# Kernel optimization log

Hardware: AMD Instinct MI355X
Metric: run time of the kernel (lower is better)

## Reference

```python
import jax, jax.numpy as jnp
import numpy as np
from math import sqrt

B, L, H, DK = 4, 2048, 16, 64


def setup_inputs() -> dict:
    key = jax.random.key(0)
    kq, kk, kv = jax.random.split(key, 3)
    queries = jax.random.normal(kq, (B, L, H, DK), dtype=jnp.float32)
    keys = jax.random.normal(kk, (B, L, H, DK), dtype=jnp.float32)
    values = jax.random.normal(kv, (B, L, H, DK), dtype=jnp.float32)
    return {"queries": queries, "keys": keys, "values": values}


def reference(queries, keys, values):
    # FullAttention forward: mask_flag=True, scale=None -> 1/sqrt(dk),
    # attention_dropout=0.0 (identity), output_attention=False.
    b, l, h, dk = queries.shape
    s = values.shape[1]
    scale = 1.0 / sqrt(dk)
    # scores: [B, H, L, S]
    scores = jnp.einsum('blhd,bshd->bhls', queries, keys)
    # causal mask: upper triangle (strictly above diagonal) -> -inf
    causal = jnp.triu(jnp.ones((l, s), dtype=bool), k=1)  # [L, S]
    scores = jnp.where(causal[None, None, :, :], -jnp.inf, scores)
    attn = jax.nn.softmax(scores * scale, axis=-1)
    out = jnp.einsum('bhls,bshd->blhd', attn, values)
    return out
```

## Files before the change

kernel.cpp:

```cpp
#include <hip/hip_runtime.h>
#include <hip/hip_bf16.h>
#include <cstdint>
#include <cstddef>

#define B_ 4
#define L_ 2048
#define H_ 16
#define D_ 64
#define BH_ (B_*H_)

typedef __attribute__((ext_vector_type(8))) short short8;
typedef __attribute__((ext_vector_type(4))) short short4_t;
typedef __attribute__((ext_vector_type(4))) float f32x4;

__device__ __forceinline__ short f2bf(float x) {
    union { float f; unsigned u; } v; v.f = x;
    unsigned r = v.u + 0x7fffu + ((v.u >> 16) & 1u);
    return (short)(r >> 16);
}

__device__ __forceinline__ short8 pack8(float4 a, float4 b, float sc) {
    short8 t;
    t[0] = f2bf(a.x * sc); t[1] = f2bf(a.y * sc);
    t[2] = f2bf(a.z * sc); t[3] = f2bf(a.w * sc);
    t[4] = f2bf(b.x * sc); t[5] = f2bf(b.y * sc);
    t[6] = f2bf(b.z * sc); t[7] = f2bf(b.w * sc);
    return t;
}

__device__ __forceinline__ float fast_exp2(float x) {
#if __has_builtin(__builtin_amdgcn_exp2f)
    return __builtin_amdgcn_exp2f(x);
#else
    return exp2f(x);
#endif
}

__device__ __forceinline__ void gld16(const void* g, void* l) {
    __builtin_amdgcn_global_load_lds(
        (const __attribute__((address_space(1))) void*)g,
        (__attribute__((address_space(3))) void*)l, 16, 0, 0);
}

__global__ __launch_bounds__(256) void prepack(
    const float* __restrict__ K, const float* __restrict__ V,
    short* __restrict__ Kb, short* __restrict__ Vt)
{
    const int blk = blockIdx.x;
    const int bh  = blk >> 5;
    const int s0  = (blk & 31) * 64;
    const int b   = bh >> 4, h = bh & 15;
    const int t   = threadIdx.x;
    __shared__ short Ls[64 * 72];

#pragma unroll
    for (int half = 0; half < 2; ++half) {
        const int sl = (t >> 3) + half * 32;
        const int dc = (t & 7) * 8;
        const size_t src_off = ((size_t)((b * L_ + s0 + sl) * H_ + h)) * D_ + dc;
        float4 f0 = *(const float4*)(K + src_off);
        float4 f1 = *(const float4*)(K + src_off + 4);
        *(short8*)&Kb[((size_t)bh * L_ + s0 + sl) * D_ + dc] = pack8(f0, f1, 1.0f);
        float4 g0 = *(const float4*)(V + src_off);
        float4 g1 = *(const float4*)(V + src_off + 4);
        *(short8*)&Ls[sl * 72 + dc] = pack8(g0, g1, 1.0f);
    }
    __syncthreads();
    const int d  = t >> 2;
    const int sc = (t & 3) * 16;
    short8 o0, o1;
#pragma unroll
    for (int j = 0; j < 8; ++j) o0[j] = Ls[(sc + j) * 72 + d];
#pragma unroll
    for (int j = 0; j < 8; ++j) o1[j] = Ls[(sc + 8 + j) * 72 + d];
    short* dst = Vt + ((size_t)bh * D_ + d) * L_ + s0 + sc;
    *(short8*)dst = o0;
    *(short8*)(dst + 8) = o1;
}

__global__ __launch_bounds__(256, 4) void fa_fwd2(
    const float* __restrict__ Q, const short* __restrict__ Kb,
    const short* __restrict__ Vt, float* __restrict__ O)
{
    const int tid  = threadIdx.x;
    const int wave = tid >> 6;
    const int lane = tid & 63;
    const int quad = lane >> 4;
    const int l16  = lane & 15;

    const int blk  = blockIdx.x;
    const int xcd  = blk & 7;
    const int slot = blk >> 3;
    const int bh   = xcd * 8 + (slot & 7);
    const int ip   = slot >> 3;
    const int b    = bh >> 4;
    const int h    = bh & 15;
    const int qtA  = ip;
    const int qtB  = 31 - ip;
    const int qbA  = qtA * 64;
    const int qbB  = qtB * 64;
    const int nkt  = qtB + 1;

    __shared__ short Ks[2][64 * 64];
    __shared__ short Vs[2][64 * 64];
    __shared__ short Ps[4][16 * 64];
    short* Pl = Ps[wave];

    const float scq = 0.125f * 1.44269504f;
    short8 qfA[2], qfB[2];
    {
        const float* qa = Q + ((size_t)((b * L_ + qbA + wave * 16 + l16) * H_ + h)) * D_;
        const float* qb = Q + ((size_t)((b * L_ + qbB + wave * 16 + l16) * H_ + h)) * D_;
#pragma unroll
        for (int kk = 0; kk < 2; ++kk) {
            const int d0 = kk * 32 + quad * 8;
            qfA[kk] = pack8(*(const float4*)(qa + d0), *(const float4*)(qa + d0 + 4), scq);
            qfB[kk] = pack8(*(const float4*)(qb + d0), *(const float4*)(qb + d0 + 4), scq);
        }
    }

    const short* Kg = Kb + (size_t)bh * L_ * D_;
    const short* Vg = Vt + (size_t)bh * D_ * L_;
    const int r8 = lane >> 3;
    const int g8 = ((lane & 7) ^ r8) * 8;

    f32x4 accA[4], accB[4];
#pragma unroll
    for (int c = 0; c < 4; ++c) {
        accA[c] = (f32x4){0.f, 0.f, 0.f, 0.f};
        accB[c] = (f32x4){0.f, 0.f, 0.f, 0.f};
    }
    float lsA[4] = {0.f, 0.f, 0.f, 0.f};
    float lsB[4] = {0.f, 0.f, 0.f, 0.f};

    auto stage = [&](int kt, int buf) {
#pragma unroll
        for (int half = 0; half < 2; ++half) {
            const int rbase = wave * 16 + half * 8;
            const int row   = rbase + r8;
            gld16(Kg + (size_t)(kt * 64 + row) * D_ + g8, &Ks[buf][rbase * 64]);
            gld16(Vg + (size_t)row * L_ + kt * 64 + g8, &Vs[buf][rbase * 64]);
        }
    };

    auto compute = [&](int kt, int buf, const short8* qf, int qt, f32x4* acc, float* ls) {
        f32x4 s[4];
#pragma unroll
        for (int ct = 0; ct < 4; ++ct) s[ct] = (f32x4){0.f, 0.f, 0.f, 0.f};
#pragma unroll
        for (int kk = 0; kk < 2; ++kk) {
            const int cs = ((kk * 4 + quad) ^ (l16 & 7)) * 8;
#pragma unroll
            for (int ct = 0; ct < 4; ++ct) {
                short8 kf = *(short8*)&Ks[buf][(ct * 16 + l16) * 64 + cs];
                s[ct] = __builtin_amdgcn_mfma_f32_16x16x32_bf16(qf[kk], kf, s[ct], 0, 0, 0);
            }
        }
        const bool diag = (kt == qt);
#pragma unroll
        for (int ct = 0; ct < 4; ++ct) {
#pragma unroll
            for (int r = 0; r < 4; ++r) {
                float sv = s[ct][r];
                if (diag && (ct * 16 + l16 > wave * 16 + quad * 4 + r)) sv = -1e30f;
                const float p = fast_exp2(sv);
                ls[r] += p;
                const int row = quad * 4 + r, col = ct * 16 + l16;
                Pl[row * 64 + ((col >> 3) ^ (row & 7)) * 8 + (col & 7)] = f2bf(p);
            }
        }
#pragma unroll
        for (int ks = 0; ks < 2; ++ks) {
            const int cs = ((ks * 4 + quad) ^ (l16 & 7)) * 8;
            short8 pa = *(short8*)&Pl[l16 * 64 + cs];
#pragma unroll
            for (int cd = 0; cd < 4; ++cd) {
                short8 vb = *(short8*)&Vs[buf][(cd * 16 + l16) * 64 + cs];
                acc[cd] = __builtin_amdgcn_mfma_f32_16x16x32_bf16(pa, vb, acc[cd], 0, 0, 0);
            }
        }
    };

    stage(0, 0);
    __syncthreads();
    for (int kt = 0; kt < nkt; ++kt) {
        const int buf = kt & 1;
        if (kt + 1 < nkt) stage(kt + 1, buf ^ 1);
        if (kt <= qtA) compute(kt, buf, qfA, qtA, accA, lsA);
        compute(kt, buf, qfB, qtB, accB, lsB);
        __syncthreads();
    }

    auto epi = [&](int qbX, f32x4* acc, float* ls) {
#pragma unroll
        for (int r = 0; r < 4; ++r) {
            float t = ls[r];
#pragma unroll
            for (int off = 1; off < 16; off <<= 1) t += __shfl_xor(t, off);
            const float inv = 1.0f / t;
            float* orow = O + ((size_t)((b * L_ + qbX + wave * 16 + quad * 4 + r) * H_ + h)) * D_ + l16;
#pragma unroll
            for (int cd = 0; cd < 4; ++cd) orow[cd * 16] = acc[cd][r] * inv;
        }
    };
    epi(qbA, accA, lsA);
    epi(qbB, accB, lsB);
}

constexpr int KS = 72;
constexpr int VS = 72;
constexpr int PS = 68;

__global__ __launch_bounds__(256) void fa_fwd(
    const float* __restrict__ Q, const float* __restrict__ K,
    const float* __restrict__ V, float* __restrict__ O)
{
    const int tid  = threadIdx.x;
    const int wave = tid >> 6;
    const int lane = tid & 63;
    const int quad = lane >> 4;
    const int l16  = lane & 15;

    const int blk  = blockIdx.x;
    const int xcd  = blk & 7;
    const int slot = blk >> 3;
    const int bh   = xcd * 8 + (slot >> 5);
    const int qtile = 31 - (slot & 31);
    const int h = bh % H_;
    const int b = bh / H_;
    const int qbase = qtile * 64;
    const int qw    = qbase + wave * 16;

    __shared__ short Ks_s[64 * KS];
    __shared__ short Vt_s[64 * VS];
    __shared__ short Ps_s[4 * 16 * PS];
    short* Pl = &Ps_s[wave * 16 * PS];

    const float* qrow = Q + ((size_t)(b * L_ + qw + l16) * H_ + h) * D_;
    short8 qf[2];
#pragma unroll
    for (int kk = 0; kk < 2; ++kk) {
        const int d0 = kk * 32 + quad * 8;
        float4 f0 = *(const float4*)(qrow + d0);
        float4 f1 = *(const float4*)(qrow + d0 + 4);
        qf[kk] = pack8(f0, f1, 0.125f * 1.44269504f);
    }

    const int ksrow = tid >> 3;
    const int kscg  = (tid & 7) * 8;
    const int vs0   = (tid >> 4) * 4;
    const int vc0   = (tid & 15) * 4;

    f32x4 acc[4];
#pragma unroll
    for (int c = 0; c < 4; ++c) acc[c] = (f32x4){0.f, 0.f, 0.f, 0.f};
    float lsum[4] = {0.f, 0.f, 0.f, 0.f};

    const int nkt = qbase / 64 + 1;

    for (int kt = 0; kt < nkt; ++kt) {
        const int kbase = kt * 64;
        __syncthreads();
#pragma unroll
        for (int half = 0; half < 2; ++half) {
            const int row = ksrow + half * 32;
            const float* kr = K + ((size_t)(b * L_ + kbase + row) * H_ + h) * D_ + kscg;
            float4 f0 = *(const float4*)kr;
            float4 f1 = *(const float4*)(kr + 4);
            *(short8*)&Ks_s[row * KS + kscg] = pack8(f0, f1, 1.0f);
        }
        {
            const float* vb0 = V + ((size_t)(b * L_ + kbase + vs0) * H_ + h) * D_ + vc0;
            float4 r0 = *(const float4*)(vb0);
            float4 r1 = *(const float4*)(vb0 + H_ * D_);
            float4 r2 = *(const float4*)(vb0 + 2 * H_ * D_);
            float4 r3 = *(const float4*)(vb0 + 3 * H_ * D_);
            short4_t w;
            w[0] = f2bf(r0.x); w[1] = f2bf(r1.x); w[2] = f2bf(r2.x); w[3] = f2bf(r3.x);
            *(short4_t*)&Vt_s[(vc0 + 0) * VS + vs0] = w;
            w[0] = f2bf(r0.y); w[1] = f2bf(r1.y); w[2] = f2bf(r2.y); w[3] = f2bf(r3.y);
            *(short4_t*)&Vt_s[(vc0 + 1) * VS + vs0] = w;
            w[0] = f2bf(r0.z); w[1] = f2bf(r1.z); w[2] = f2bf(r2.z); w[3] = f2bf(r3.z);
            *(short4_t*)&Vt_s[(vc0 + 2) * VS + vs0] = w;
            w[0] = f2bf(r0.w); w[1] = f2bf(r1.w); w[2] = f2bf(r2.w); w[3] = f2bf(r3.w);
            *(short4_t*)&Vt_s[(vc0 + 3) * VS + vs0] = w;
        }
        __syncthreads();

        f32x4 s[4];
#pragma unroll
        for (int ct = 0; ct < 4; ++ct) s[ct] = (f32x4){0.f, 0.f, 0.f, 0.f};
#pragma unroll
        for (int kk = 0; kk < 2; ++kk) {
#pragma unroll
            for (int ct = 0; ct < 4; ++ct) {
                short8 kf = *(short8*)&Ks_s[(ct * 16 + l16) * KS + kk * 32 + quad * 8];
                s[ct] = __builtin_amdgcn_mfma_f32_16x16x32_bf16(qf[kk], kf, s[ct], 0, 0, 0);
            }
        }
        const bool diag = (kbase == qbase);
#pragma unroll
        for (int ct = 0; ct < 4; ++ct) {
#pragma unroll
            for (int r = 0; r < 4; ++r) {
                float sv = s[ct][r];
                if (diag && (ct * 16 + l16 > wave * 16 + quad * 4 + r)) sv = -1e30f;
                float p = fast_exp2(sv);
                lsum[r] += p;
                Pl[(quad * 4 + r) * PS + ct * 16 + l16] = f2bf(p);
            }
        }
#pragma unroll
        for (int ks = 0; ks < 2; ++ks) {
            short8 pa = *(short8*)&Pl[l16 * PS + ks * 32 + quad * 8];
#pragma unroll
            for (int c = 0; c < 4; ++c) {
                short8 vb = *(short8*)&Vt_s[(c * 16 + l16) * VS + ks * 32 + quad * 8];
                acc[c] = __builtin_amdgcn_mfma_f32_16x16x32_bf16(pa, vb, acc[c], 0, 0, 0);
            }
        }
    }

#pragma unroll
    for (int r = 0; r < 4; ++r) {
        float t = lsum[r];
#pragma unroll
        for (int off = 1; off < 16; off <<= 1) t += __shfl_xor(t, off);
        const float inv = 1.0f / t;
        const size_t row_off = ((size_t)(b * L_ + qw + quad * 4 + r) * H_ + h) * D_;
#pragma unroll
        for (int c = 0; c < 4; ++c)
            O[row_off + c * 16 + l16] = acc[c][r] * inv;
    }
}

extern "C" void kernel_launch(void* const* d_in, const int* in_sizes, int n_in,
                              void* d_out, int out_size, void* d_ws, size_t ws_size,
                              hipStream_t stream) {
    const float* Q = (const float*)d_in[0];
    const float* K = (const float*)d_in[1];
    const float* V = (const float*)d_in[2];
    float* O = (float*)d_out;
    const size_t need = (size_t)2 * BH_ * L_ * D_ * sizeof(short);
    if (ws_size >= need) {
        short* Kb = (short*)d_ws;
        short* Vt = Kb + (size_t)BH_ * L_ * D_;
        prepack<<<dim3(BH_ * (L_ / 64)), dim3(256), 0, stream>>>(K, V, Kb, Vt);
        fa_fwd2<<<dim3(1024), dim3(256), 0, stream>>>(Q, Kb, Vt, O);
    } else {
        fa_fwd<<<dim3(B_ * H_ * (L_ / 64)), dim3(256), 0, stream>>>(Q, K, V, O);
    }
}
```

Baseline: 187.7 us.

## Pack P as bf16 pairs in LDS and byte-permute into MFMA operands

Instead of writing each probability as a separate 16-bit LDS store with an XOR swizzle, each lane packs two rows' values into one 32-bit word and writes them into a row-pair layout. The PV A-operand is read back as two 16-byte loads and rearranged with v_perm into the required short8. V fragments are now loaded for both k-steps before the MFMAs. This cuts the number of LDS store instructions and overlaps the V loads, at the cost of extra perm ALU work, more registers, and a changed conversion routine (__float2bfloat16).

```diff
diff --git a/kernel.cpp b/kernel.cpp
--- a/kernel.cpp
+++ b/kernel.cpp
@@ -11,6 +11,7 @@
 
 typedef __attribute__((ext_vector_type(8))) short short8;
 typedef __attribute__((ext_vector_type(4))) short short4_t;
+typedef __attribute__((ext_vector_type(4))) unsigned uint4_t;
 typedef __attribute__((ext_vector_type(4))) float f32x4;
 
 __device__ __forceinline__ short f2bf(float x) {
@@ -34,6 +35,12 @@
 #else
     return exp2f(x);
 #endif
+}
+
+__device__ __forceinline__ unsigned pack_bf2(float a, float b) {
+    unsigned lo = __bfloat16_as_ushort(__float2bfloat16(a));
+    unsigned hi = __bfloat16_as_ushort(__float2bfloat16(b));
+    return lo | (hi << 16);
 }
 
 __device__ __forceinline__ void gld16(const void* g, void* l) {
@@ -103,8 +110,12 @@
 
     __shared__ short Ks[2][64 * 64];
     __shared__ short Vs[2][64 * 64];
-    __shared__ short Ps[4][16 * 64];
-    short* Pl = Ps[wave];
+    __shared__ unsigned P2s[4][512];
+    unsigned* Pw = P2s[wave];
+    unsigned* p2w0 = Pw + (quad * 2) * 64 + l16;
+    unsigned* p2w1 = Pw + (quad * 2 + 1) * 64 + l16;
+    const unsigned* p2r = Pw + (l16 >> 1) * 64 + quad * 8;
+    const unsigned psel = (l16 & 1) ? 0x07060302u : 0x05040100u;
 
     const float scq = 0.125f * 1.44269504f;
     short8 qfA[2], qfB[2];
@@ -159,25 +170,38 @@
         const bool diag = (kt == qt);
 #pragma unroll
         for (int ct = 0; ct < 4; ++ct) {
+            float p[4];
 #pragma unroll
             for (int r = 0; r < 4; ++r) {
                 float sv = s[ct][r];
                 if (diag && (ct * 16 + l16 > wave * 16 + quad * 4 + r)) sv = -1e30f;
-                const float p = fast_exp2(sv);
-                ls[r] += p;
-                const int row = quad * 4 + r, col = ct * 16 + l16;
-                Pl[row * 64 + ((col >> 3) ^ (row & 7)) * 8 + (col & 7)] = f2bf(p);
-            }
-        }
+                p[r] = fast_exp2(sv);
+                ls[r] += p[r];
+            }
+            p2w0[ct * 16] = pack_bf2(p[0], p[1]);
+            p2w1[ct * 16] = pack_bf2(p[2], p[3]);
+        }
+        short8 vbr[2][4];
 #pragma unroll
         for (int ks = 0; ks < 2; ++ks) {
             const int cs = ((ks * 4 + quad) ^ (l16 & 7)) * 8;
-            short8 pa = *(short8*)&Pl[l16 * 64 + cs];
-#pragma unroll
-            for (int cd = 0; cd < 4; ++cd) {
-                short8 vb = *(short8*)&Vs[buf][(cd * 16 + l16) * 64 + cs];
-                acc[cd] = __builtin_amdgcn_mfma_f32_16x16x32_bf16(pa, vb, acc[cd], 0, 0, 0);
-            }
+#pragma unroll
+            for (int cd = 0; cd < 4; ++cd)
+                vbr[ks][cd] = *(short8*)&Vs[buf][(cd * 16 + l16) * 64 + cs];
+        }
+#pragma unroll
+        for (int ks = 0; ks < 2; ++ks) {
+            uint4_t a0 = *(const uint4_t*)(p2r + ks * 32);
+            uint4_t a1 = *(const uint4_t*)(p2r + ks * 32 + 4);
+            uint4_t w;
+            w[0] = __builtin_amdgcn_perm(a0[1], a0[0], psel);
+            w[1] = __builtin_amdgcn_perm(a0[3], a0[2], psel);
+            w[2] = __builtin_amdgcn_perm(a1[1], a1[0], psel);
+            w[3] = __builtin_amdgcn_perm(a1[3], a1[2], psel);
+            short8 pa = *(short8*)&w;
+#pragma unroll
+            for (int cd = 0; cd < 4; ++cd)
+                acc[cd] = __builtin_amdgcn_mfma_f32_16x16x32_bf16(pa, vbr[ks][cd], acc[cd], 0, 0, 0);
         }
     };
 
```

Result: no change. 190.8 us (+1.7%).

## Split paired query tiles across waves so each wave owns 32 rows

Applied to the files above, without the earlier changes.

Work is redistributed so waves 0-1 handle the short query tile A and waves 2-3 handle the long tile B, each wave covering 32 query rows. Before, every wave processed 16 rows of both tiles. Each K/V fragment read from LDS now feeds two MFMAs, and s_setprio is raised around the MFMA sections. The cost is load imbalance: the A-tile waves go idle after their diagonal but still hit the barriers. The kernel also uses more registers and a larger P buffer, so the occupancy hint drops to 3 blocks per SIMD group.

```diff
diff --git a/kernel.cpp b/kernel.cpp
--- a/kernel.cpp
+++ b/kernel.cpp
@@ -78,7 +78,7 @@
     *(short8*)(dst + 8) = o1;
 }
 
-__global__ __launch_bounds__(256, 4) void fa_fwd2(
+__global__ __launch_bounds__(256, 3) void fa_fwd2(
     const float* __restrict__ Q, const short* __restrict__ Kb,
     const short* __restrict__ Vt, float* __restrict__ O)
 {
@@ -97,25 +97,27 @@
     const int h    = bh & 15;
     const int qtA  = ip;
     const int qtB  = 31 - ip;
-    const int qbA  = qtA * 64;
-    const int qbB  = qtB * 64;
     const int nkt  = qtB + 1;
+
+    const int qt   = (wave < 2) ? qtA : qtB;
+    const int qoff = (wave & 1) * 32;
+    const int rbw  = qt * 64 + qoff;
 
     __shared__ short Ks[2][64 * 64];
     __shared__ short Vs[2][64 * 64];
-    __shared__ short Ps[4][16 * 64];
+    __shared__ short Ps[4][32 * 64];
     short* Pl = Ps[wave];
 
     const float scq = 0.125f * 1.44269504f;
-    short8 qfA[2], qfB[2];
+    short8 qf0[2], qf1[2];
     {
-        const float* qa = Q + ((size_t)((b * L_ + qbA + wave * 16 + l16) * H_ + h)) * D_;
-        const float* qb = Q + ((size_t)((b * L_ + qbB + wave * 16 + l16) * H_ + h)) * D_;
+        const float* qa = Q + ((size_t)((b * L_ + rbw + l16) * H_ + h)) * D_;
+        const float* qb = Q + ((size_t)((b * L_ + rbw + 16 + l16) * H_ + h)) * D_;
 #pragma unroll
         for (int kk = 0; kk < 2; ++kk) {
             const int d0 = kk * 32 + quad * 8;
-            qfA[kk] = pack8(*(const float4*)(qa + d0), *(const float4*)(qa + d0 + 4), scq);
-            qfB[kk] = pack8(*(const float4*)(qb + d0), *(const float4*)(qb + d0 + 4), scq);
+            qf0[kk] = pack8(*(const float4*)(qa + d0), *(const float4*)(qa + d0 + 4), scq);
+            qf1[kk] = pack8(*(const float4*)(qb + d0), *(const float4*)(qb + d0 + 4), scq);
         }
     }
 
@@ -124,14 +126,14 @@
     const int r8 = lane >> 3;
     const int g8 = ((lane & 7) ^ r8) * 8;
 
-    f32x4 accA[4], accB[4];
+    f32x4 acc0[4], acc1[4];
 #pragma unroll
     for (int c = 0; c < 4; ++c) {
-        accA[c] = (f32x4){0.f, 0.f, 0.f, 0.f};
-        accB[c] = (f32x4){0.f, 0.f, 0.f, 0.f};
-    }
-    float lsA[4] = {0.f, 0.f, 0.f, 0.f};
-    float lsB[4] = {0.f, 0.f, 0.f, 0.f};
+        acc0[c] = (f32x4){0.f, 0.f, 0.f, 0.f};
+        acc1[c] = (f32x4){0.f, 0.f, 0.f, 0.f};
+    }
+    float ls0[4] = {0.f, 0.f, 0.f, 0.f};
+    float ls1[4] = {0.f, 0.f, 0.f, 0.f};
 
     auto stage = [&](int kt, int buf) {
 #pragma unroll
@@ -143,42 +145,64 @@
         }
     };
 
-    auto compute = [&](int kt, int buf, const short8* qf, int qt, f32x4* acc, float* ls) {
-        f32x4 s[4];
-#pragma unroll
-        for (int ct = 0; ct < 4; ++ct) s[ct] = (f32x4){0.f, 0.f, 0.f, 0.f};
+    auto compute = [&](int kt, int buf) {
+        f32x4 s0[4], s1[4];
+#pragma unroll
+        for (int ct = 0; ct < 4; ++ct) {
+            s0[ct] = (f32x4){0.f, 0.f, 0.f, 0.f};
+            s1[ct] = (f32x4){0.f, 0.f, 0.f, 0.f};
+        }
+        __builtin_amdgcn_s_setprio(1);
 #pragma unroll
         for (int kk = 0; kk < 2; ++kk) {
             const int cs = ((kk * 4 + quad) ^ (l16 & 7)) * 8;
 #pragma unroll
             for (int ct = 0; ct < 4; ++ct) {
                 short8 kf = *(short8*)&Ks[buf][(ct * 16 + l16) * 64 + cs];
-                s[ct] = __builtin_amdgcn_mfma_f32_16x16x32_bf16(qf[kk], kf, s[ct], 0, 0, 0);
-            }
-        }
+                s0[ct] = __builtin_amdgcn_mfma_f32_16x16x32_bf16(qf0[kk], kf, s0[ct], 0, 0, 0);
+                s1[ct] = __builtin_amdgcn_mfma_f32_16x16x32_bf16(qf1[kk], kf, s1[ct], 0, 0, 0);
+            }
+        }
+        __builtin_amdgcn_s_setprio(0);
         const bool diag = (kt == qt);
 #pragma unroll
         for (int ct = 0; ct < 4; ++ct) {
 #pragma unroll
             for (int r = 0; r < 4; ++r) {
-                float sv = s[ct][r];
-                if (diag && (ct * 16 + l16 > wave * 16 + quad * 4 + r)) sv = -1e30f;
+                float sv = s0[ct][r];
+                if (diag && (ct * 16 + l16 > qoff + quad * 4 + r)) sv = -1e30f;
                 const float p = fast_exp2(sv);
-                ls[r] += p;
+                ls0[r] += p;
                 const int row = quad * 4 + r, col = ct * 16 + l16;
                 Pl[row * 64 + ((col >> 3) ^ (row & 7)) * 8 + (col & 7)] = f2bf(p);
             }
         }
 #pragma unroll
+        for (int ct = 0; ct < 4; ++ct) {
+#pragma unroll
+            for (int r = 0; r < 4; ++r) {
+                float sv = s1[ct][r];
+                if (diag && (ct * 16 + l16 > qoff + 16 + quad * 4 + r)) sv = -1e30f;
+                const float p = fast_exp2(sv);
+                ls1[r] += p;
+                const int row = 16 + quad * 4 + r, col = ct * 16 + l16;
+                Pl[row * 64 + ((col >> 3) ^ (row & 7)) * 8 + (col & 7)] = f2bf(p);
+            }
+        }
+        __builtin_amdgcn_s_setprio(1);
+#pragma unroll
         for (int ks = 0; ks < 2; ++ks) {
             const int cs = ((ks * 4 + quad) ^ (l16 & 7)) * 8;
-            short8 pa = *(short8*)&Pl[l16 * 64 + cs];
+            short8 pa0 = *(short8*)&Pl[l16 * 64 + cs];
+            short8 pa1 = *(short8*)&Pl[(16 + l16) * 64 + cs];
 #pragma unroll
             for (int cd = 0; cd < 4; ++cd) {
                 short8 vb = *(short8*)&Vs[buf][(cd * 16 + l16) * 64 + cs];
-                acc[cd] = __builtin_amdgcn_mfma_f32_16x16x32_bf16(pa, vb, acc[cd], 0, 0, 0);
-            }
-        }
+                acc0[cd] = __builtin_amdgcn_mfma_f32_16x16x32_bf16(pa0, vb, acc0[cd], 0, 0, 0);
+                acc1[cd] = __builtin_amdgcn_mfma_f32_16x16x32_bf16(pa1, vb, acc1[cd], 0, 0, 0);
+            }
+        }
+        __builtin_amdgcn_s_setprio(0);
     };
 
     stage(0, 0);
@@ -186,25 +210,24 @@
     for (int kt = 0; kt < nkt; ++kt) {
         const int buf = kt & 1;
         if (kt + 1 < nkt) stage(kt + 1, buf ^ 1);
-        if (kt <= qtA) compute(kt, buf, qfA, qtA, accA, lsA);
-        compute(kt, buf, qfB, qtB, accB, lsB);
+        if (kt <= qt) compute(kt, buf);
         __syncthreads();
     }
 
-    auto epi = [&](int qbX, f32x4* acc, float* ls) {
+    auto epi = [&](int rg, f32x4* acc, float* ls) {
 #pragma unroll
         for (int r = 0; r < 4; ++r) {
             float t = ls[r];
 #pragma unroll
             for (int off = 1; off < 16; off <<= 1) t += __shfl_xor(t, off);
             const float inv = 1.0f / t;
-            float* orow = O + ((size_t)((b * L_ + qbX + wave * 16 + quad * 4 + r) * H_ + h)) * D_ + l16;
+            float* orow = O + ((size_t)((b * L_ + rbw + rg * 16 + quad * 4 + r) * H_ + h)) * D_ + l16;
 #pragma unroll
             for (int cd = 0; cd < 4; ++cd) orow[cd * 16] = acc[cd][r] * inv;
         }
     };
-    epi(qbA, accA, lsA);
-    epi(qbB, accB, lsB);
+    epi(0, acc0, ls0);
+    epi(1, acc1, ls1);
 }
 
 constexpr int KS = 72;
```

Measured after the change: 221.1 us. +17.8%, slower.
